# Optimization experiments

Hardware: AMD Instinct MI355X
Metric: run time of the kernel (lower is better)

## Reference

```python
import jax, jax.numpy as jnp
import numpy as np

NLAYER = 4
H = 0.1


def tv_norm(X, eps=1e-3):
    # mean-center and L2-normalize each channel over the node/edge dim
    X = X - jnp.mean(X, axis=1, keepdims=True)
    return X / jnp.sqrt(jnp.sum(X * X, axis=1, keepdims=True) + eps)


def setup_inputs() -> dict:
    key = jax.random.key(0)
    ks = jax.random.split(key, 12)
    nIn, nopenN, nopenE, nclose = 128, 128, 128, 128
    nN, nE = 50000, 500000
    xn = jax.random.normal(ks[0], (nIn, nN), dtype=jnp.float32)
    xe = jax.random.normal(ks[1], (nIn, nE), dtype=jnp.float32)
    iInd = jax.random.randint(ks[2], (nE,), 0, nN)
    jInd = jax.random.randint(ks[3], (nE,), 0, nN)
    KNopen = jax.random.uniform(ks[4], (nopenN, nIn), dtype=jnp.float32) * 0.1
    KEopen = jax.random.uniform(ks[5], (nopenE, nIn), dtype=jnp.float32) * 0.1
    KNclose = jax.random.uniform(ks[6], (nclose, nopenN), dtype=jnp.float32) * 0.1
    KEclose = jax.random.uniform(ks[7], (nclose, nopenE), dtype=jnp.float32) * 0.1
    KN = jax.random.uniform(ks[8], (NLAYER, nopenE, nopenN), dtype=jnp.float32) * 0.001
    KE = jax.random.uniform(ks[9], (NLAYER, nopenN, nopenE), dtype=jnp.float32) * 0.001
    return {"xn": xn, "xe": xe, "iInd": iInd, "jInd": jInd,
            "KNopen": KNopen, "KEopen": KEopen, "KNclose": KNclose,
            "KEclose": KEclose, "KN": KN, "KE": KE}


def reference(xn, xe, iInd, jInd, KNopen, KEopen, KNclose, KEclose, KN, KE):
    nN = xn.shape[1]

    def node_grad(x):           # [d, nN] -> [d, nE]
        return x[:, iInd] - x[:, jInd]

    def edge_div(e):            # [d, nE] -> [d, nN]
        z = jnp.zeros((e.shape[0], nN), dtype=e.dtype)
        return z.at[:, iInd].add(e).at[:, jInd].add(-e)

    xn = KNopen @ xn            # [nopenN, nN]
    xe = KEopen @ xe            # [nopenE, nE]
    for i in range(NLAYER):
        Ai = tv_norm(KN[i] @ node_grad(xn))          # [nopenE, nE]
        xe = xe + H * jax.nn.relu(Ai)
        Bi = tv_norm(jax.nn.relu(KE[i] @ edge_div(xe)))  # [nopenN, nN]
        xn = xn + H * jax.nn.relu(Bi)
    xn = KNclose @ xn
    xe = KNclose @ xe  # note: original code uses KNclose for xe as well
    return (xn, xe)
```

## Files before the change

### kernel.cpp

```cpp
#include <hip/hip_runtime.h>


#define HSTEP 0.1f
#define TVEPS 1e-3f

typedef __attribute__((ext_vector_type(8))) short short8v;
typedef __attribute__((ext_vector_type(4))) float f32x4;

__device__ inline float4 f4z() { return make_float4(0.f, 0.f, 0.f, 0.f); }

__device__ inline unsigned short f2bf(float x) {
  unsigned u = __float_as_uint(x);
  unsigned r = (u + 0x7fffu + ((u >> 16) & 1u)) >> 16;
  return (unsigned short)r;
}
__device__ inline float bf2f(unsigned short h) {
  return __uint_as_float(((unsigned)h) << 16);
}

__global__ __launch_bounds__(256, 2) void gemm_e(
    const float* __restrict__ X, const float* __restrict__ Kmat, const int N,
    float* __restrict__ Yt) {
  __shared__ float Xs[32 * 68];
  __shared__ float Ks[32 * 132];
  const int tid = threadIdx.x;
  const int ng = tid & 15, og = tid >> 4;
  const long e0 = (long)blockIdx.x * 64;

  float acc[4][8];
#pragma unroll
  for (int q = 0; q < 4; ++q)
#pragma unroll
    for (int j = 0; j < 8; ++j) acc[q][j] = 0.f;

  for (int kc = 0; kc < 128; kc += 32) {
#pragma unroll
    for (int i = 0; i < 2; ++i) {
      int f4i = tid + 256 * i;
      int kk = f4i >> 4, e4 = (f4i & 15) << 2;
      long ge = e0 + e4;
      float4 v = f4z();
      if (ge + 3 < N) {
        v = *(const float4*)&X[(long)(kc + kk) * N + ge];
      } else {
        float* pv = &v.x;
        for (int q = 0; q < 4; ++q)
          if (ge + q < N) pv[q] = X[(long)(kc + kk) * N + ge + q];
      }
      *(float4*)&Xs[kk * 68 + e4] = v;
    }
#pragma unroll
    for (int i = 0; i < 4; ++i) {
      int f4i = tid + 256 * i;
      int o = f4i >> 3, c4 = (f4i & 7) << 2;
      float4 v = *(const float4*)&Kmat[o * 128 + kc + c4];
      Ks[(c4 + 0) * 132 + o] = v.x;
      Ks[(c4 + 1) * 132 + o] = v.y;
      Ks[(c4 + 2) * 132 + o] = v.z;
      Ks[(c4 + 3) * 132 + o] = v.w;
    }
    __syncthreads();
#pragma unroll
    for (int kk = 0; kk < 32; ++kk) {
      const float4 xq = *(const float4*)&Xs[kk * 68 + 4 * ng];
      const float4 k0 = *(const float4*)&Ks[kk * 132 + 8 * og];
      const float4 k1 = *(const float4*)&Ks[kk * 132 + 8 * og + 4];
      float xv[4] = {xq.x, xq.y, xq.z, xq.w};
      float kv[8] = {k0.x, k0.y, k0.z, k0.w, k1.x, k1.y, k1.z, k1.w};
#pragma unroll
      for (int q = 0; q < 4; ++q)
#pragma unroll
        for (int j = 0; j < 8; ++j) acc[q][j] = fmaf(xv[q], kv[j], acc[q][j]);
    }
    __syncthreads();
  }

#pragma unroll
  for (int q = 0; q < 4; ++q) {
    long e = e0 + 4 * ng + q;
    if (e < N) {
      *(float4*)&Yt[e * 128 + 8 * og] =
          make_float4(acc[q][0], acc[q][1], acc[q][2], acc[q][3]);
      *(float4*)&Yt[e * 128 + 8 * og + 4] =
          make_float4(acc[q][4], acc[q][5], acc[q][6], acc[q][7]);
    }
  }
}

template <int MODE>
__global__ __launch_bounds__(256, 2) void gemm_n(
    const float* __restrict__ X, const float* __restrict__ Kmat, const int N,
    float* __restrict__ Y, float* __restrict__ statS,
    float* __restrict__ statQ) {
  __shared__ float Xs[64 * 33];
  __shared__ float Ks[32 * 132];
  __shared__ float red[(MODE == 1) ? 2 * 128 * 17 : 4];
  const int tid = threadIdx.x;
  const int ng = tid & 15, og = tid >> 4;
  const long n0 = (long)blockIdx.x * 64;

  float acc[4][8];
#pragma unroll
  for (int q = 0; q < 4; ++q)
#pragma unroll
    for (int j = 0; j < 8; ++j) acc[q][j] = 0.f;

  for (int kc = 0; kc < 128; kc += 32) {
#pragma unroll
    for (int i = 0; i < 2; ++i) {
      int f4i = tid + 256 * i;
      int n = f4i >> 3, c4 = (f4i & 7) << 2;
      long gn = n0 + n;
      float4 v = f4z();
      if (gn < N) v = *(const float4*)&X[gn * 128 + kc + c4];
      Xs[n * 33 + c4 + 0] = v.x;
      Xs[n * 33 + c4 + 1] = v.y;
      Xs[n * 33 + c4 + 2] = v.z;
      Xs[n * 33 + c4 + 3] = v.w;
    }
#pragma unroll
    for (int i = 0; i < 4; ++i) {
      int f4i = tid + 256 * i;
      int o = f4i >> 3, c4 = (f4i & 7) << 2;
      float4 v = *(const float4*)&Kmat[o * 128 + kc + c4];
      Ks[(c4 + 0) * 132 + o] = v.x;
      Ks[(c4 + 1) * 132 + o] = v.y;
      Ks[(c4 + 2) * 132 + o] = v.z;
      Ks[(c4 + 3) * 132 + o] = v.w;
    }
    __syncthreads();
#pragma unroll
    for (int kk = 0; kk < 32; ++kk) {
      float xv[4];
#pragma unroll
      for (int q = 0; q < 4; ++q) xv[q] = Xs[(4 * ng + q) * 33 + kk];
      const float4 k0 = *(const float4*)&Ks[kk * 132 + 8 * og];
      const float4 k1 = *(const float4*)&Ks[kk * 132 + 8 * og + 4];
      float kv[8] = {k0.x, k0.y, k0.z, k0.w, k1.x, k1.y, k1.z, k1.w};
#pragma unroll
      for (int q = 0; q < 4; ++q)
#pragma unroll
        for (int j = 0; j < 8; ++j) acc[q][j] = fmaf(xv[q], kv[j], acc[q][j]);
    }
    __syncthreads();
  }

  if (MODE == 0) {
#pragma unroll
    for (int q = 0; q < 4; ++q) {
      long n = n0 + 4 * ng + q;
      if (n < N) {
        *(float4*)&Y[n * 128 + 8 * og] =
            make_float4(acc[q][0], acc[q][1], acc[q][2], acc[q][3]);
        *(float4*)&Y[n * 128 + 8 * og + 4] =
            make_float4(acc[q][4], acc[q][5], acc[q][6], acc[q][7]);
      }
    }
  } else if (MODE == 1) {
#pragma unroll
    for (int q = 0; q < 4; ++q)
#pragma unroll
      for (int j = 0; j < 8; ++j) acc[q][j] = fmaxf(acc[q][j], 0.f);
#pragma unroll
    for (int q = 0; q < 4; ++q) {
      long n = n0 + 4 * ng + q;
      if (n < N) {
        *(float4*)&Y[n * 128 + 8 * og] =
            make_float4(acc[q][0], acc[q][1], acc[q][2], acc[q][3]);
        *(float4*)&Y[n * 128 + 8 * og + 4] =
            make_float4(acc[q][4], acc[q][5], acc[q][6], acc[q][7]);
      }
    }
    float* redS = red;
    float* redQ = red + 128 * 17;
#pragma unroll
    for (int j = 0; j < 8; ++j) {
      int o = 8 * og + j;
      float s = acc[0][j] + acc[1][j] + acc[2][j] + acc[3][j];
      float qq = acc[0][j] * acc[0][j] + acc[1][j] * acc[1][j] +
                 acc[2][j] * acc[2][j] + acc[3][j] * acc[3][j];
      redS[o * 17 + ng] = s;
      redQ[o * 17 + ng] = qq;
    }
    __syncthreads();
    if (tid < 128) {
      float s = 0.f, qq = 0.f;
#pragma unroll
      for (int g = 0; g < 16; ++g) {
        s += redS[tid * 17 + g];
        qq += redQ[tid * 17 + g];
      }
      atomicAdd(&statS[tid], s);
      atomicAdd(&statQ[tid], qq);
    }
  } else {
    long n = n0 + 4 * ng;
#pragma unroll
    for (int j = 0; j < 8; ++j) {
      long o = 8 * og + j;
      float4 v = make_float4(acc[0][j], acc[1][j], acc[2][j], acc[3][j]);
      if (n + 3 < N) {
        *(float4*)&Y[o * N + n] = v;
      } else {
        const float* pv = &v.x;
        for (int q = 0; q < 4; ++q)
          if (n + q < N) Y[o * N + n + q] = pv[q];
      }
    }
  }
}

__global__ __launch_bounds__(256) void prep_close_w(
    const float* __restrict__ KNclose, const float* __restrict__ KEopen,
    unsigned short* __restrict__ Apack) {
  const int idx = blockIdx.x * 256 + threadIdx.x;
  const int p = idx >> 14, ok = idx & 16383;
  const int o = ok >> 7, k = ok & 127;
  float val;
  if (p == 0) {
    float s = 0.f;
    for (int m = 0; m < 128; ++m)
      s = fmaf(KNclose[o * 128 + m], KEopen[m * 128 + k], s);
    val = s;
  } else {
    val = KNclose[o * 128 + k];
  }
  const unsigned short hi = f2bf(val);
  const unsigned short lo = f2bf(val - bf2f(hi));
  const int chunk = p * 4 + (k >> 5);
  const int lane = (o & 15) + 16 * ((k >> 3) & 3);
  const int base = chunk * 8192 + (o >> 4) * 512 + lane * 8 + (k & 7);
  Apack[base] = hi;
  Apack[base + 4096] = lo;
}

__global__ __launch_bounds__(256, 2) void close_edge_mfma(
    const float* __restrict__ xe, const float* __restrict__ Sacc,
    const unsigned short* __restrict__ Apack, const int nE,
    float* __restrict__ out) {
  __shared__ float4 Asf[1024];
  const int tid = threadIdx.x;
  const int l = tid & 63, w = tid >> 6;
  const int er = l & 15;
  const int kg = l >> 4;
  const long e0 = (long)blockIdx.x * 128;

  f32x4 acc[8][2];
#pragma unroll
  for (int of = 0; of < 8; ++of)
#pragma unroll
    for (int f = 0; f < 2; ++f) acc[of][f] = (f32x4){0.f, 0.f, 0.f, 0.f};

  long e_f[2];
  bool ev[2];
#pragma unroll
  for (int f = 0; f < 2; ++f) {
    long e = e0 + 32 * w + 16 * f + er;
    ev[f] = (e < nE);
    e_f[f] = ev[f] ? e : (long)(nE - 1);
  }

  const short8v* Ap = (const short8v*)Asf;

  for (int p = 0; p < 2; ++p) {
    for (int ks = 0; ks < 4; ++ks) {
      const float4* src = (const float4*)Apack + (p * 4 + ks) * 1024;
      __syncthreads();
      Asf[tid] = src[tid];
      Asf[tid + 256] = src[tid + 256];
      Asf[tid + 512] = src[tid + 512];
      Asf[tid + 768] = src[tid + 768];
      __syncthreads();

      short8v bh[2], bl[2];
#pragma unroll
      for (int f = 0; f < 2; ++f) {
        float xv[8];
        if (p == 0) {
          const float* col = xe + e_f[f];
          const int kbase = 32 * ks + 8 * kg;
#pragma unroll
          for (int j = 0; j < 8; ++j) xv[j] = col[(long)(kbase + j) * nE];
        } else {
          const float* row = Sacc + e_f[f] * 128 + 32 * ks + 8 * kg;
          const float4 v0 = *(const float4*)row;
          const float4 v1 = *(const float4*)(row + 4);
          xv[0] = v0.x; xv[1] = v0.y; xv[2] = v0.z; xv[3] = v0.w;
          xv[4] = v1.x; xv[5] = v1.y; xv[6] = v1.z; xv[7] = v1.w;
        }
#pragma unroll
        for (int j = 0; j < 8; ++j) {
          const unsigned short h = f2bf(xv[j]);
          const unsigned short lo = f2bf(xv[j] - bf2f(h));
          bh[f][j] = (short)h;
          bl[f][j] = (short)lo;
        }
      }

#pragma unroll
      for (int of = 0; of < 8; ++of) {
        const short8v ah = Ap[of * 64 + l];
        const short8v al = Ap[512 + of * 64 + l];
#pragma unroll
        for (int f = 0; f < 2; ++f) {
          acc[of][f] =
              __builtin_amdgcn_mfma_f32_16x16x32_bf16(ah, bh[f], acc[of][f], 0, 0, 0);
          acc[of][f] =
              __builtin_amdgcn_mfma_f32_16x16x32_bf16(ah, bl[f], acc[of][f], 0, 0, 0);
          acc[of][f] =
              __builtin_amdgcn_mfma_f32_16x16x32_bf16(al, bh[f], acc[of][f], 0, 0, 0);
        }
      }
    }
  }

#pragma unroll
  for (int of = 0; of < 8; ++of) {
#pragma unroll
    for (int f = 0; f < 2; ++f) {
      if (!ev[f]) continue;
      const long e = e0 + 32 * w + 16 * f + er;
#pragma unroll
      for (int r = 0; r < 4; ++r) {
        const long o = of * 16 + 4 * kg + r;
        out[o * nE + e] = acc[of][f][r];
      }
    }
  }
}

__global__ __launch_bounds__(256) void count_deg(const int* __restrict__ iInd,
                                                 const int* __restrict__ jInd,
                                                 const int nE,
                                                 int* __restrict__ cnt) {
  const int e = blockIdx.x * 256 + threadIdx.x;
  if (e >= nE) return;
  atomicAdd(&cnt[iInd[e]], 1);
  atomicAdd(&cnt[jInd[e]], 1);
}

__global__ __launch_bounds__(1024) void scan_rowptr(const int* __restrict__ cnt,
                                                    int* __restrict__ rp,
                                                    const int nN) {
  __shared__ int buf[1024];
  __shared__ int carry;
  const int tid = threadIdx.x;
  if (tid == 0) {
    carry = 0;
    rp[0] = 0;
  }
  __syncthreads();
  for (int base = 0; base < nN; base += 1024) {
    int idx = base + tid;
    int v = (idx < nN) ? cnt[idx] : 0;
    buf[tid] = v;
    __syncthreads();
    for (int off = 1; off < 1024; off <<= 1) {
      int t = (tid >= off) ? buf[tid - off] : 0;
      __syncthreads();
      buf[tid] += t;
      __syncthreads();
    }
    if (idx < nN) rp[idx + 1] = buf[tid] + carry;
    __syncthreads();
    if (tid == 0) carry += buf[1023];
    __syncthreads();
  }
}

__global__ __launch_bounds__(256) void fill_adj(const int* __restrict__ iInd,
                                                const int* __restrict__ jInd,
                                                const int nE,
                                                const int* __restrict__ rp,
                                                int* __restrict__ cur,
                                                int* __restrict__ adj) {
  const int e = blockIdx.x * 256 + threadIdx.x;
  if (e >= nE) return;
  const int ii = iInd[e], jj = jInd[e];
  int s1 = atomicAdd(&cur[ii], 1);
  adj[rp[ii] + s1] = (e << 1);
  int s2 = atomicAdd(&cur[jj], 1);
  adj[rp[jj] + s2] = (e << 1) | 1;
}

template <bool OPEN>
__global__ __launch_bounds__(256) void div_gather(
    const float* __restrict__ E, const int* __restrict__ rp,
    const int* __restrict__ adj, const float* __restrict__ D0,
    float* __restrict__ D, const int nN) {
  const int cg = threadIdx.x & 31, slot = threadIdx.x >> 5;
  const long n = (long)blockIdx.x * 8 + slot;
  if (n >= nN) return;
  const float4* E4 = (const float4*)E;
  float4 acc;
  if (OPEN) {
    acc = f4z();
  } else {
    acc = ((const float4*)D0)[n * 32 + cg];
  }
  const int b = rp[n], en = rp[n + 1];
  for (int k = b; k < en; ++k) {
    const int ent = adj[k];
    const long e = ent >> 1;
    const float4 v = E4[e * 32 + cg];
    if (ent & 1) {
      acc.x -= v.x; acc.y -= v.y; acc.z -= v.z; acc.w -= v.w;
    } else {
      acc.x += v.x; acc.y += v.y; acc.z += v.z; acc.w += v.w;
    }
  }
  ((float4*)D)[n * 32 + cg] = acc;
}

__global__ __launch_bounds__(256) void edge_pass1(
    const float* __restrict__ W, const int* __restrict__ iInd,
    const int* __restrict__ jInd, const int nE, float* __restrict__ statS,
    float* __restrict__ statQ) {
  __shared__ float4 rs[256];
  __shared__ float4 rq[256];
  const int tid = threadIdx.x;
  const int cg = tid & 31, slot = tid >> 5;
  const float4* W4 = (const float4*)W;
  float4 s = f4z(), q = f4z();
  long start = (long)blockIdx.x * 512;
  long end = start + 512;
  if (end > nE) end = nE;
  for (long e = start + slot; e < end; e += 8) {
    const int ii = iInd[e], jj = jInd[e];
    const float4 wi = W4[(long)ii * 32 + cg];
    const float4 wj = W4[(long)jj * 32 + cg];
    const float y0 = wi.x - wj.x, y1 = wi.y - wj.y;
    const float y2 = wi.z - wj.z, y3 = wi.w - wj.w;
    s.x += y0; s.y += y1; s.z += y2; s.w += y3;
    q.x = fmaf(y0, y0, q.x); q.y = fmaf(y1, y1, q.y);
    q.z = fmaf(y2, y2, q.z); q.w = fmaf(y3, y3, q.w);
  }
  rs[tid] = s;
  rq[tid] = q;
  __syncthreads();
  if (tid < 32) {
    float4 S = rs[tid], Q = rq[tid];
#pragma unroll
    for (int g = 1; g < 8; ++g) {
      float4 a = rs[tid + 32 * g], b = rq[tid + 32 * g];
      S.x += a.x; S.y += a.y; S.z += a.z; S.w += a.w;
      Q.x += b.x; Q.y += b.y; Q.z += b.z; Q.w += b.w;
    }
    atomicAdd(&statS[tid * 4 + 0], S.x);
    atomicAdd(&statS[tid * 4 + 1], S.y);
    atomicAdd(&statS[tid * 4 + 2], S.z);
    atomicAdd(&statS[tid * 4 + 3], S.w);
    atomicAdd(&statQ[tid * 4 + 0], Q.x);
    atomicAdd(&statQ[tid * 4 + 1], Q.y);
    atomicAdd(&statQ[tid * 4 + 2], Q.z);
    atomicAdd(&statQ[tid * 4 + 3], Q.w);
  }
}

template <bool FIRST>
__global__ __launch_bounds__(256) void edge_pass2(
    const float* __restrict__ W, const int* __restrict__ iInd,
    const int* __restrict__ jInd, const int nE, const float* __restrict__ mean,
    const float* __restrict__ rsig, float* __restrict__ Sacc) {
  const int tid = threadIdx.x;
  const int cg = tid & 31, slot = tid >> 5;
  const float4 mu = *(const float4*)&mean[cg * 4];
  const float4 sg = *(const float4*)&rsig[cg * 4];
  const float4* W4 = (const float4*)W;
  float4* S4 = (float4*)Sacc;
  long start = (long)blockIdx.x * 512;
  long end = start + 512;
  if (end > nE) end = nE;
  for (long e = start + slot; e < end; e += 8) {
    const int ii = iInd[e], jj = jInd[e];
    const float4 wi = W4[(long)ii * 32 + cg];
    const float4 wj = W4[(long)jj * 32 + cg];
    const float r0 = fmaxf(((wi.x - wj.x) - mu.x) * sg.x, 0.f) * HSTEP;
    const float r1 = fmaxf(((wi.y - wj.y) - mu.y) * sg.y, 0.f) * HSTEP;
    const float r2 = fmaxf(((wi.z - wj.z) - mu.z) * sg.z, 0.f) * HSTEP;
    const float r3 = fmaxf(((wi.w - wj.w) - mu.w) * sg.w, 0.f) * HSTEP;
    float4 sv;
    if (FIRST) {
      sv = make_float4(r0, r1, r2, r3);
    } else {
      sv = S4[e * 32 + cg];
      sv.x += r0; sv.y += r1; sv.z += r2; sv.w += r3;
    }
    S4[e * 32 + cg] = sv;
  }
}

__global__ void fin_stats(const float* __restrict__ S,
                          const float* __restrict__ Q, const float cnt,
                          float* __restrict__ mean, float* __restrict__ rsig) {
  const int c = threadIdx.x;
  const float mu = S[c] / cnt;
  const float var = Q[c] - cnt * mu * mu;
  mean[c] = mu;
  rsig[c] = rsqrtf(var + TVEPS);
}

__global__ __launch_bounds__(256) void apply_node(
    const float* __restrict__ R, const float* __restrict__ mean,
    const float* __restrict__ rsig, float* __restrict__ xnt,
    const long total4) {
  const long idx = (long)blockIdx.x * 256 + threadIdx.x;
  if (idx >= total4) return;
  const int o4 = (int)(idx & 31) * 4;
  const float4 m = *(const float4*)&mean[o4];
  const float4 s = *(const float4*)&rsig[o4];
  const float4 r = ((const float4*)R)[idx];
  float4 x = ((float4*)xnt)[idx];
  x.x += HSTEP * fmaxf((r.x - m.x) * s.x, 0.f);
  x.y += HSTEP * fmaxf((r.y - m.y) * s.y, 0.f);
  x.z += HSTEP * fmaxf((r.z - m.z) * s.z, 0.f);
  x.w += HSTEP * fmaxf((r.w - m.w) * s.w, 0.f);
  ((float4*)xnt)[idx] = x;
}

extern "C" void kernel_launch(void* const* d_in, const int* in_sizes, int n_in,
                              void* d_out, int out_size, void* d_ws,
                              size_t ws_size, hipStream_t stream) {
  const float* xn = (const float*)d_in[0];
  const float* xe = (const float*)d_in[1];
  const int* iInd = (const int*)d_in[2];
  const int* jInd = (const int*)d_in[3];
  const float* KNopen = (const float*)d_in[4];
  const float* KEopen = (const float*)d_in[5];
  const float* KNclose = (const float*)d_in[6];
  const float* KN = (const float*)d_in[8];
  const float* KE = (const float*)d_in[9];

  const int nN = in_sizes[0] / 128;
  const int nE = in_sizes[2];

  float* out_xn = (float*)d_out;
  float* out_xe = (float*)d_out + (size_t)128 * nN;

  float* ws = (float*)d_ws;
  size_t off = 0;
  float* Sacc = ws + off; off += (size_t)nE * 128;
  float* W    = ws + off; off += (size_t)nN * 128;
  float* Dacc = ws + off; off += (size_t)nN * 128;
  float* D0   = ws + off; off += (size_t)nN * 128;
  float* xnt  = ws + off; off += (size_t)nN * 128;
  unsigned short* Apack = (unsigned short*)(ws + off); off += 32768;
  float* stats = ws + off; off += 1024;
  float* statS = stats;        float* statQ = stats + 128;
  float* meanE = stats + 256;  float* rsigE = stats + 384;
  float* statS2 = stats + 512; float* statQ2 = stats + 640;
  float* meanN = stats + 768;  float* rsigN = stats + 896;
  int* rp  = (int*)(ws + off); off += (size_t)nN + 1 + 63;
  int* cnt = (int*)(ws + off); off += nN;
  int* cur = (int*)(ws + off); off += nN;
  int* adj = (int*)(ws + off); off += (size_t)2 * nE;
  float* Eopen = Sacc;
  float* R = W;

  const int gN = (nN + 63) / 64;
  const int gE = (nE + 63) / 64;
  const int gEm = (nE + 127) / 128;
  const int gP = (nE + 511) / 512;
  const int gEdge = (nE + 255) / 256;
  const int gGath = (nN + 7) / 8;
  const int gA = (int)(((long)nN * 32 + 255) / 256);

  hipMemsetAsync(cnt, 0, (size_t)nN * sizeof(int), stream);
  hipMemsetAsync(cur, 0, (size_t)nN * sizeof(int), stream);
  count_deg<<<gEdge, 256, 0, stream>>>(iInd, jInd, nE, cnt);
  scan_rowptr<<<1, 1024, 0, stream>>>(cnt, rp, nN);
  fill_adj<<<gEdge, 256, 0, stream>>>(iInd, jInd, nE, rp, cur, adj);

  gemm_e<<<gN, 256, 0, stream>>>(xn, KNopen, nN, xnt);
  gemm_e<<<gE, 256, 0, stream>>>(xe, KEopen, nE, Eopen);
  prep_close_w<<<128, 256, 0, stream>>>(KNclose, KEopen, Apack);
  div_gather<true><<<gGath, 256, 0, stream>>>(Eopen, rp, adj, nullptr, D0, nN);

  for (int layer = 0; layer < 4; ++layer) {
    hipMemsetAsync(stats, 0, 1024 * sizeof(float), stream);
    gemm_n<0><<<gN, 256, 0, stream>>>(xnt, KN + layer * 16384, nN, W, nullptr,
                                      nullptr);
    edge_pass1<<<gP, 256, 0, stream>>>(W, iInd, jInd, nE, statS, statQ);
    fin_stats<<<1, 128, 0, stream>>>(statS, statQ, (float)nE, meanE, rsigE);
    if (layer == 0)
      edge_pass2<true><<<gP, 256, 0, stream>>>(W, iInd, jInd, nE, meanE, rsigE,
                                               Sacc);
    else
      edge_pass2<false><<<gP, 256, 0, stream>>>(W, iInd, jInd, nE, meanE,
                                                rsigE, Sacc);
    div_gather<false><<<gGath, 256, 0, stream>>>(Sacc, rp, adj, D0, Dacc, nN);
    gemm_n<1><<<gN, 256, 0, stream>>>(Dacc, KE + layer * 16384, nN, R, statS2,
                                      statQ2);
    fin_stats<<<1, 128, 0, stream>>>(statS2, statQ2, (float)nN, meanN, rsigN);
    apply_node<<<gA, 256, 0, stream>>>(R, meanN, rsigN, xnt, (long)nN * 32);
  }

  gemm_n<2><<<gN, 256, 0, stream>>>(xnt, KNclose, nN, out_xn, nullptr,
                                    nullptr);
  close_edge_mfma<<<gEm, 256, 0, stream>>>(xe, Sacc, Apack, nE, out_xe);
}
```

Before: 3.153 ms.

## Move open, node-layer and close GEMMs to split-bf16 MFMA kernels

Replaces the scalar-FMA fp32 GEMMs for the opening projections, the per-layer KN node GEMM and the closing node GEMM with MFMA kernels. These use bf16x3 emulation (hi/lo splits of weights and activations, three MFMAs per product). A new pack6 kernel pre-packs the weights into MFMA lane layout. The large xe opening GEMM (500k edges) is the main target, trading FMA throughput for matrix-core throughput at some accuracy cost from dropping the lo*lo term. The KE GEMM with its stats epilogue stays on the scalar path, and the close_edge indexing is tweaked to reuse the clamped index.

```diff
diff --git a/kernel.cpp b/kernel.cpp
--- a/kernel.cpp
+++ b/kernel.cpp
@@ -18,196 +18,25 @@
   return __uint_as_float(((unsigned)h) << 16);
 }
 
-__global__ __launch_bounds__(256, 2) void gemm_e(
-    const float* __restrict__ X, const float* __restrict__ Kmat, const int N,
-    float* __restrict__ Yt) {
-  __shared__ float Xs[32 * 68];
-  __shared__ float Ks[32 * 132];
-  const int tid = threadIdx.x;
-  const int ng = tid & 15, og = tid >> 4;
-  const long e0 = (long)blockIdx.x * 64;
-
-  float acc[4][8];
-#pragma unroll
-  for (int q = 0; q < 4; ++q)
-#pragma unroll
-    for (int j = 0; j < 8; ++j) acc[q][j] = 0.f;
-
-  for (int kc = 0; kc < 128; kc += 32) {
-#pragma unroll
-    for (int i = 0; i < 2; ++i) {
-      int f4i = tid + 256 * i;
-      int kk = f4i >> 4, e4 = (f4i & 15) << 2;
-      long ge = e0 + e4;
-      float4 v = f4z();
-      if (ge + 3 < N) {
-        v = *(const float4*)&X[(long)(kc + kk) * N + ge];
-      } else {
-        float* pv = &v.x;
-        for (int q = 0; q < 4; ++q)
-          if (ge + q < N) pv[q] = X[(long)(kc + kk) * N + ge + q];
-      }
-      *(float4*)&Xs[kk * 68 + e4] = v;
-    }
-#pragma unroll
-    for (int i = 0; i < 4; ++i) {
-      int f4i = tid + 256 * i;
-      int o = f4i >> 3, c4 = (f4i & 7) << 2;
-      float4 v = *(const float4*)&Kmat[o * 128 + kc + c4];
-      Ks[(c4 + 0) * 132 + o] = v.x;
-      Ks[(c4 + 1) * 132 + o] = v.y;
-      Ks[(c4 + 2) * 132 + o] = v.z;
-      Ks[(c4 + 3) * 132 + o] = v.w;
-    }
-    __syncthreads();
-#pragma unroll
-    for (int kk = 0; kk < 32; ++kk) {
-      const float4 xq = *(const float4*)&Xs[kk * 68 + 4 * ng];
-      const float4 k0 = *(const float4*)&Ks[kk * 132 + 8 * og];
-      const float4 k1 = *(const float4*)&Ks[kk * 132 + 8 * og + 4];
-      float xv[4] = {xq.x, xq.y, xq.z, xq.w};
-      float kv[8] = {k0.x, k0.y, k0.z, k0.w, k1.x, k1.y, k1.z, k1.w};
-#pragma unroll
-      for (int q = 0; q < 4; ++q)
-#pragma unroll
-        for (int j = 0; j < 8; ++j) acc[q][j] = fmaf(xv[q], kv[j], acc[q][j]);
-    }
-    __syncthreads();
-  }
-
-#pragma unroll
-  for (int q = 0; q < 4; ++q) {
-    long e = e0 + 4 * ng + q;
-    if (e < N) {
-      *(float4*)&Yt[e * 128 + 8 * og] =
-          make_float4(acc[q][0], acc[q][1], acc[q][2], acc[q][3]);
-      *(float4*)&Yt[e * 128 + 8 * og + 4] =
-          make_float4(acc[q][4], acc[q][5], acc[q][6], acc[q][7]);
-    }
-  }
-}
-
-template <int MODE>
-__global__ __launch_bounds__(256, 2) void gemm_n(
-    const float* __restrict__ X, const float* __restrict__ Kmat, const int N,
-    float* __restrict__ Y, float* __restrict__ statS,
-    float* __restrict__ statQ) {
-  __shared__ float Xs[64 * 33];
-  __shared__ float Ks[32 * 132];
-  __shared__ float red[(MODE == 1) ? 2 * 128 * 17 : 4];
-  const int tid = threadIdx.x;
-  const int ng = tid & 15, og = tid >> 4;
-  const long n0 = (long)blockIdx.x * 64;
-
-  float acc[4][8];
-#pragma unroll
-  for (int q = 0; q < 4; ++q)
-#pragma unroll
-    for (int j = 0; j < 8; ++j) acc[q][j] = 0.f;
-
-  for (int kc = 0; kc < 128; kc += 32) {
-#pragma unroll
-    for (int i = 0; i < 2; ++i) {
-      int f4i = tid + 256 * i;
-      int n = f4i >> 3, c4 = (f4i & 7) << 2;
-      long gn = n0 + n;
-      float4 v = f4z();
-      if (gn < N) v = *(const float4*)&X[gn * 128 + kc + c4];
-      Xs[n * 33 + c4 + 0] = v.x;
-      Xs[n * 33 + c4 + 1] = v.y;
-      Xs[n * 33 + c4 + 2] = v.z;
-      Xs[n * 33 + c4 + 3] = v.w;
-    }
-#pragma unroll
-    for (int i = 0; i < 4; ++i) {
-      int f4i = tid + 256 * i;
-      int o = f4i >> 3, c4 = (f4i & 7) << 2;
-      float4 v = *(const float4*)&Kmat[o * 128 + kc + c4];
-      Ks[(c4 + 0) * 132 + o] = v.x;
-      Ks[(c4 + 1) * 132 + o] = v.y;
-      Ks[(c4 + 2) * 132 + o] = v.z;
-      Ks[(c4 + 3) * 132 + o] = v.w;
-    }
-    __syncthreads();
-#pragma unroll
-    for (int kk = 0; kk < 32; ++kk) {
-      float xv[4];
-#pragma unroll
-      for (int q = 0; q < 4; ++q) xv[q] = Xs[(4 * ng + q) * 33 + kk];
-      const float4 k0 = *(const float4*)&Ks[kk * 132 + 8 * og];
-      const float4 k1 = *(const float4*)&Ks[kk * 132 + 8 * og + 4];
-      float kv[8] = {k0.x, k0.y, k0.z, k0.w, k1.x, k1.y, k1.z, k1.w};
-#pragma unroll
-      for (int q = 0; q < 4; ++q)
-#pragma unroll
-        for (int j = 0; j < 8; ++j) acc[q][j] = fmaf(xv[q], kv[j], acc[q][j]);
-    }
-    __syncthreads();
-  }
-
-  if (MODE == 0) {
-#pragma unroll
-    for (int q = 0; q < 4; ++q) {
-      long n = n0 + 4 * ng + q;
-      if (n < N) {
-        *(float4*)&Y[n * 128 + 8 * og] =
-            make_float4(acc[q][0], acc[q][1], acc[q][2], acc[q][3]);
-        *(float4*)&Y[n * 128 + 8 * og + 4] =
-            make_float4(acc[q][4], acc[q][5], acc[q][6], acc[q][7]);
-      }
-    }
-  } else if (MODE == 1) {
-#pragma unroll
-    for (int q = 0; q < 4; ++q)
-#pragma unroll
-      for (int j = 0; j < 8; ++j) acc[q][j] = fmaxf(acc[q][j], 0.f);
-#pragma unroll
-    for (int q = 0; q < 4; ++q) {
-      long n = n0 + 4 * ng + q;
-      if (n < N) {
-        *(float4*)&Y[n * 128 + 8 * og] =
-            make_float4(acc[q][0], acc[q][1], acc[q][2], acc[q][3]);
-        *(float4*)&Y[n * 128 + 8 * og + 4] =
-            make_float4(acc[q][4], acc[q][5], acc[q][6], acc[q][7]);
-      }
-    }
-    float* redS = red;
-    float* redQ = red + 128 * 17;
-#pragma unroll
-    for (int j = 0; j < 8; ++j) {
-      int o = 8 * og + j;
-      float s = acc[0][j] + acc[1][j] + acc[2][j] + acc[3][j];
-      float qq = acc[0][j] * acc[0][j] + acc[1][j] * acc[1][j] +
-                 acc[2][j] * acc[2][j] + acc[3][j] * acc[3][j];
-      redS[o * 17 + ng] = s;
-      redQ[o * 17 + ng] = qq;
-    }
-    __syncthreads();
-    if (tid < 128) {
-      float s = 0.f, qq = 0.f;
-#pragma unroll
-      for (int g = 0; g < 16; ++g) {
-        s += redS[tid * 17 + g];
-        qq += redQ[tid * 17 + g];
-      }
-      atomicAdd(&statS[tid], s);
-      atomicAdd(&statQ[tid], qq);
-    }
-  } else {
-    long n = n0 + 4 * ng;
-#pragma unroll
-    for (int j = 0; j < 8; ++j) {
-      long o = 8 * og + j;
-      float4 v = make_float4(acc[0][j], acc[1][j], acc[2][j], acc[3][j]);
-      if (n + 3 < N) {
-        *(float4*)&Y[o * N + n] = v;
-      } else {
-        const float* pv = &v.x;
-        for (int q = 0; q < 4; ++q)
-          if (n + q < N) Y[o * N + n + q] = pv[q];
-      }
-    }
-  }
+__global__ __launch_bounds__(256) void pack6(const float* __restrict__ KNopen,
+                                             const float* __restrict__ KEopen,
+                                             const float* __restrict__ KN,
+                                             unsigned short* __restrict__ dst) {
+  const int idx = blockIdx.x * 256 + threadIdx.x;
+  const int m = blockIdx.y;
+  const int o = idx >> 7, k = idx & 127;
+  const float* src;
+  if (m == 0) src = KNopen;
+  else if (m == 1) src = KEopen;
+  else src = KN + (m - 2) * 16384;
+  const float val = src[o * 128 + k];
+  const unsigned short hi = f2bf(val);
+  const unsigned short lo = f2bf(val - bf2f(hi));
+  const int lane = (o & 15) + 16 * ((k >> 3) & 3);
+  const int base =
+      m * 32768 + (k >> 5) * 8192 + (o >> 4) * 512 + lane * 8 + (k & 7);
+  dst[base] = hi;
+  dst[base + 4096] = lo;
 }
 
 __global__ __launch_bounds__(256) void prep_close_w(
@@ -234,6 +63,272 @@
   Apack[base + 4096] = lo;
 }
 
+__global__ __launch_bounds__(256, 2) void gemm_e_mfma(
+    const float* __restrict__ X, const unsigned short* __restrict__ Wp,
+    const int N, float* __restrict__ Yt) {
+  __shared__ float4 Asf[1024];
+  const int tid = threadIdx.x;
+  const int l = tid & 63, w = tid >> 6;
+  const int er = l & 15, kg = l >> 4;
+  const long e0 = (long)blockIdx.x * 128;
+
+  f32x4 acc[8][2];
+#pragma unroll
+  for (int of = 0; of < 8; ++of)
+#pragma unroll
+    for (int f = 0; f < 2; ++f) acc[of][f] = (f32x4){0.f, 0.f, 0.f, 0.f};
+
+  long e_f[2];
+  bool ev[2];
+#pragma unroll
+  for (int f = 0; f < 2; ++f) {
+    long e = e0 + 32 * w + 16 * f + er;
+    ev[f] = (e < N);
+    e_f[f] = ev[f] ? e : (long)(N - 1);
+  }
+
+  const short8v* Ap = (const short8v*)Asf;
+
+  for (int ks = 0; ks < 4; ++ks) {
+    const float4* src = (const float4*)Wp + ks * 1024;
+    __syncthreads();
+    Asf[tid] = src[tid];
+    Asf[tid + 256] = src[tid + 256];
+    Asf[tid + 512] = src[tid + 512];
+    Asf[tid + 768] = src[tid + 768];
+    __syncthreads();
+
+    short8v bh[2], bl[2];
+#pragma unroll
+    for (int f = 0; f < 2; ++f) {
+      const float* col = X + e_f[f];
+      const int kbase = 32 * ks + 8 * kg;
+      float xv[8];
+#pragma unroll
+      for (int j = 0; j < 8; ++j) xv[j] = col[(long)(kbase + j) * N];
+#pragma unroll
+      for (int j = 0; j < 8; ++j) {
+        const unsigned short h = f2bf(xv[j]);
+        const unsigned short lo = f2bf(xv[j] - bf2f(h));
+        bh[f][j] = (short)h;
+        bl[f][j] = (short)lo;
+      }
+    }
+
+#pragma unroll
+    for (int of = 0; of < 8; ++of) {
+      const short8v ah = Ap[of * 64 + l];
+      const short8v al = Ap[512 + of * 64 + l];
+#pragma unroll
+      for (int f = 0; f < 2; ++f) {
+        acc[of][f] =
+            __builtin_amdgcn_mfma_f32_16x16x32_bf16(ah, bh[f], acc[of][f], 0, 0, 0);
+        acc[of][f] =
+            __builtin_amdgcn_mfma_f32_16x16x32_bf16(ah, bl[f], acc[of][f], 0, 0, 0);
+        acc[of][f] =
+            __builtin_amdgcn_mfma_f32_16x16x32_bf16(al, bh[f], acc[of][f], 0, 0, 0);
+      }
+    }
+  }
+
+#pragma unroll
+  for (int of = 0; of < 8; ++of) {
+#pragma unroll
+    for (int f = 0; f < 2; ++f) {
+      if (!ev[f]) continue;
+      *(f32x4*)&Yt[e_f[f] * 128 + of * 16 + 4 * kg] = acc[of][f];
+    }
+  }
+}
+
+template <int MODE>
+__global__ __launch_bounds__(256, 2) void gemm_n_mfma(
+    const float* __restrict__ X, const unsigned short* __restrict__ Wp,
+    const int N, float* __restrict__ Y) {
+  __shared__ float4 Asf[1024];
+  const int tid = threadIdx.x;
+  const int l = tid & 63, w = tid >> 6;
+  const int er = l & 15, kg = l >> 4;
+  const long n0 = (long)blockIdx.x * 128;
+
+  f32x4 acc[8][2];
+#pragma unroll
+  for (int of = 0; of < 8; ++of)
+#pragma unroll
+    for (int f = 0; f < 2; ++f) acc[of][f] = (f32x4){0.f, 0.f, 0.f, 0.f};
+
+  long n_f[2];
+  bool nv[2];
+#pragma unroll
+  for (int f = 0; f < 2; ++f) {
+    long n = n0 + 32 * w + 16 * f + er;
+    nv[f] = (n < N);
+    n_f[f] = nv[f] ? n : (long)(N - 1);
+  }
+
+  const short8v* Ap = (const short8v*)Asf;
+
+  for (int ks = 0; ks < 4; ++ks) {
+    const float4* src = (const float4*)Wp + ks * 1024;
+    __syncthreads();
+    Asf[tid] = src[tid];
+    Asf[tid + 256] = src[tid + 256];
+    Asf[tid + 512] = src[tid + 512];
+    Asf[tid + 768] = src[tid + 768];
+    __syncthreads();
+
+    short8v bh[2], bl[2];
+#pragma unroll
+    for (int f = 0; f < 2; ++f) {
+      const float* row = X + n_f[f] * 128 + 32 * ks + 8 * kg;
+      const float4 v0 = *(const float4*)row;
+      const float4 v1 = *(const float4*)(row + 4);
+      float xv[8] = {v0.x, v0.y, v0.z, v0.w, v1.x, v1.y, v1.z, v1.w};
+#pragma unroll
+      for (int j = 0; j < 8; ++j) {
+        const unsigned short h = f2bf(xv[j]);
+        const unsigned short lo = f2bf(xv[j] - bf2f(h));
+        bh[f][j] = (short)h;
+        bl[f][j] = (short)lo;
+      }
+    }
+
+#pragma unroll
+    for (int of = 0; of < 8; ++of) {
+      const short8v ah = Ap[of * 64 + l];
+      const short8v al = Ap[512 + of * 64 + l];
+#pragma unroll
+      for (int f = 0; f < 2; ++f) {
+        acc[of][f] =
+            __builtin_amdgcn_mfma_f32_16x16x32_bf16(ah, bh[f], acc[of][f], 0, 0, 0);
+        acc[of][f] =
+            __builtin_amdgcn_mfma_f32_16x16x32_bf16(ah, bl[f], acc[of][f], 0, 0, 0);
+        acc[of][f] =
+            __builtin_amdgcn_mfma_f32_16x16x32_bf16(al, bh[f], acc[of][f], 0, 0, 0);
+      }
+    }
+  }
+
+  if (MODE == 0) {
+#pragma unroll
+    for (int of = 0; of < 8; ++of) {
+#pragma unroll
+      for (int f = 0; f < 2; ++f) {
+        if (!nv[f]) continue;
+        *(f32x4*)&Y[n_f[f] * 128 + of * 16 + 4 * kg] = acc[of][f];
+      }
+    }
+  } else {
+#pragma unroll
+    for (int of = 0; of < 8; ++of) {
+#pragma unroll
+      for (int f = 0; f < 2; ++f) {
+        if (!nv[f]) continue;
+#pragma unroll
+        for (int r = 0; r < 4; ++r) {
+          const long o = of * 16 + 4 * kg + r;
+          Y[o * N + n_f[f]] = acc[of][f][r];
+        }
+      }
+    }
+  }
+}
+
+__global__ __launch_bounds__(256, 2) void gemm_n1(
+    const float* __restrict__ X, const float* __restrict__ Kmat, const int N,
+    float* __restrict__ Y, float* __restrict__ statS,
+    float* __restrict__ statQ) {
+  __shared__ float Xs[64 * 33];
+  __shared__ float Ks[32 * 132];
+  __shared__ float red[2 * 128 * 17];
+  const int tid = threadIdx.x;
+  const int ng = tid & 15, og = tid >> 4;
+  const long n0 = (long)blockIdx.x * 64;
+
+  float acc[4][8];
+#pragma unroll
+  for (int q = 0; q < 4; ++q)
+#pragma unroll
+    for (int j = 0; j < 8; ++j) acc[q][j] = 0.f;
+
+  for (int kc = 0; kc < 128; kc += 32) {
+#pragma unroll
+    for (int i = 0; i < 2; ++i) {
+      int f4i = tid + 256 * i;
+      int n = f4i >> 3, c4 = (f4i & 7) << 2;
+      long gn = n0 + n;
+      float4 v = f4z();
+      if (gn < N) v = *(const float4*)&X[gn * 128 + kc + c4];
+      Xs[n * 33 + c4 + 0] = v.x;
+      Xs[n * 33 + c4 + 1] = v.y;
+      Xs[n * 33 + c4 + 2] = v.z;
+      Xs[n * 33 + c4 + 3] = v.w;
+    }
+#pragma unroll
+    for (int i = 0; i < 4; ++i) {
+      int f4i = tid + 256 * i;
+      int o = f4i >> 3, c4 = (f4i & 7) << 2;
+      float4 v = *(const float4*)&Kmat[o * 128 + kc + c4];
+      Ks[(c4 + 0) * 132 + o] = v.x;
+      Ks[(c4 + 1) * 132 + o] = v.y;
+      Ks[(c4 + 2) * 132 + o] = v.z;
+      Ks[(c4 + 3) * 132 + o] = v.w;
+    }
+    __syncthreads();
+#pragma unroll
+    for (int kk = 0; kk < 32; ++kk) {
+      float xv[4];
+#pragma unroll
+      for (int q = 0; q < 4; ++q) xv[q] = Xs[(4 * ng + q) * 33 + kk];
+      const float4 k0 = *(const float4*)&Ks[kk * 132 + 8 * og];
+      const float4 k1 = *(const float4*)&Ks[kk * 132 + 8 * og + 4];
+      float kv[8] = {k0.x, k0.y, k0.z, k0.w, k1.x, k1.y, k1.z, k1.w};
+#pragma unroll
+      for (int q = 0; q < 4; ++q)
+#pragma unroll
+        for (int j = 0; j < 8; ++j) acc[q][j] = fmaf(xv[q], kv[j], acc[q][j]);
+    }
+    __syncthreads();
+  }
+
+#pragma unroll
+  for (int q = 0; q < 4; ++q)
+#pragma unroll
+    for (int j = 0; j < 8; ++j) acc[q][j] = fmaxf(acc[q][j], 0.f);
+#pragma unroll
+  for (int q = 0; q < 4; ++q) {
+    long n = n0 + 4 * ng + q;
+    if (n < N) {
+      *(float4*)&Y[n * 128 + 8 * og] =
+          make_float4(acc[q][0], acc[q][1], acc[q][2], acc[q][3]);
+      *(float4*)&Y[n * 128 + 8 * og + 4] =
+          make_float4(acc[q][4], acc[q][5], acc[q][6], acc[q][7]);
+    }
+  }
+  float* redS = red;
+  float* redQ = red + 128 * 17;
+#pragma unroll
+  for (int j = 0; j < 8; ++j) {
+    int o = 8 * og + j;
+    float s = acc[0][j] + acc[1][j] + acc[2][j] + acc[3][j];
+    float qq = acc[0][j] * acc[0][j] + acc[1][j] * acc[1][j] +
+               acc[2][j] * acc[2][j] + acc[3][j] * acc[3][j];
+    redS[o * 17 + ng] = s;
+    redQ[o * 17 + ng] = qq;
+  }
+  __syncthreads();
+  if (tid < 128) {
+    float s = 0.f, qq = 0.f;
+#pragma unroll
+    for (int g = 0; g < 16; ++g) {
+      s += redS[tid * 17 + g];
+      qq += redQ[tid * 17 + g];
+    }
+    atomicAdd(&statS[tid], s);
+    atomicAdd(&statQ[tid], qq);
+  }
+}
+
 __global__ __launch_bounds__(256, 2) void close_edge_mfma(
     const float* __restrict__ xe, const float* __restrict__ Sacc,
     const unsigned short* __restrict__ Apack, const int nE,
@@ -319,7 +414,7 @@
 #pragma unroll
     for (int f = 0; f < 2; ++f) {
       if (!ev[f]) continue;
-      const long e = e0 + 32 * w + 16 * f + er;
+      const long e = e_f[f];
 #pragma unroll
       for (int r = 0; r < 4; ++r) {
         const long o = of * 16 + 4 * kg + r;
@@ -545,6 +640,7 @@
   float* D0   = ws + off; off += (size_t)nN * 128;
   float* xnt  = ws + off; off += (size_t)nN * 128;
   unsigned short* Apack = (unsigned short*)(ws + off); off += 32768;
+  unsigned short* Wpack = (unsigned short*)(ws + off); off += 98304;
   float* stats = ws + off; off += 1024;
   float* statS = stats;        float* statQ = stats + 128;
   float* meanE = stats + 256;  float* rsigE = stats + 384;
@@ -558,7 +654,7 @@
   float* R = W;
 
   const int gN = (nN + 63) / 64;
-  const int gE = (nE + 63) / 64;
+  const int gNm = (nN + 127) / 128;
   const int gEm = (nE + 127) / 128;
   const int gP = (nE + 511) / 512;
   const int gEdge = (nE + 255) / 256;
@@ -571,15 +667,17 @@
   scan_rowptr<<<1, 1024, 0, stream>>>(cnt, rp, nN);
   fill_adj<<<gEdge, 256, 0, stream>>>(iInd, jInd, nE, rp, cur, adj);
 
-  gemm_e<<<gN, 256, 0, stream>>>(xn, KNopen, nN, xnt);
-  gemm_e<<<gE, 256, 0, stream>>>(xe, KEopen, nE, Eopen);
+  pack6<<<dim3(64, 6), 256, 0, stream>>>(KNopen, KEopen, KN, Wpack);
   prep_close_w<<<128, 256, 0, stream>>>(KNclose, KEopen, Apack);
+
+  gemm_e_mfma<<<gNm, 256, 0, stream>>>(xn, Wpack, nN, xnt);
+  gemm_e_mfma<<<gEm, 256, 0, stream>>>(xe, Wpack + 32768, nE, Eopen);
   div_gather<true><<<gGath, 256, 0, stream>>>(Eopen, rp, adj, nullptr, D0, nN);
 
   for (int layer = 0; layer < 4; ++layer) {
     hipMemsetAsync(stats, 0, 1024 * sizeof(float), stream);
-    gemm_n<0><<<gN, 256, 0, stream>>>(xnt, KN + layer * 16384, nN, W, nullptr,
-                                      nullptr);
+    gemm_n_mfma<0><<<gNm, 256, 0, stream>>>(
+        xnt, Wpack + (size_t)(2 + layer) * 32768, nN, W);
     edge_pass1<<<gP, 256, 0, stream>>>(W, iInd, jInd, nE, statS, statQ);
     fin_stats<<<1, 128, 0, stream>>>(statS, statQ, (float)nE, meanE, rsigE);
     if (layer == 0)
@@ -589,13 +687,12 @@
       edge_pass2<false><<<gP, 256, 0, stream>>>(W, iInd, jInd, nE, meanE,
                                                 rsigE, Sacc);
     div_gather<false><<<gGath, 256, 0, stream>>>(Sacc, rp, adj, D0, Dacc, nN);
-    gemm_n<1><<<gN, 256, 0, stream>>>(Dacc, KE + layer * 16384, nN, R, statS2,
-                                      statQ2);
+    gemm_n1<<<gN, 256, 0, stream>>>(Dacc, KE + layer * 16384, nN, R, statS2,
+                                    statQ2);
     fin_stats<<<1, 128, 0, stream>>>(statS2, statQ2, (float)nN, meanN, rsigN);
     apply_node<<<gA, 256, 0, stream>>>(R, meanN, rsigN, xnt, (long)nN * 32);
   }
 
-  gemm_n<2><<<gN, 256, 0, stream>>>(xnt, KNclose, nN, out_xn, nullptr,
-                                    nullptr);
+  gemm_n_mfma<2><<<gNm, 256, 0, stream>>>(xnt, Apack + 32768, nN, out_xn);
   close_edge_mfma<<<gEm, 256, 0, stream>>>(xe, Sacc, Apack, nE, out_xe);
 }
```

Result: faster. 2.979 ms (-5.5%).
